# Kernel tuning notes

Measured on AMD Instinct MI355X. Metric: run time of the kernel, lower is better.

The kernel has to match this reference:

```python
import jax, jax.numpy as jnp
import numpy as np

M, U, H, C, EMB, HID = 4096, 8, 8, 64, 64, 128
N = M * U            # 32768 nodes
E = 131072           # edges
D = H * C            # 512 = heads * hidden_channels
NUM_LAYERS = 4
IN0 = 6              # 2 coords + mask + speed + cost + arrival
SCALE = np.float32(1.0 / np.sqrt(C))

def _lin(x, W, b):
    return x @ W + b

def _transformer_conv(x, src, dst, Wq, bq, Wk, bk, Wv, bv, Ws, bs):
    # PyG TransformerConv: x_j = x[src], x_i = x[dst]; softmax over edges per dst
    n = x.shape[0]
    q = _lin(x, Wq, bq).reshape(n, H, C)
    k = _lin(x, Wk, bk).reshape(n, H, C)
    v = _lin(x, Wv, bv).reshape(n, H, C)
    alpha = jnp.einsum('ehc,ehc->eh', q[dst], k[src]) * SCALE   # [E,H]
    amax = jax.ops.segment_max(alpha, dst, num_segments=n)       # [N,H]
    ex = jnp.exp(alpha - amax[dst])
    denom = jax.ops.segment_sum(ex, dst, num_segments=n)         # [N,H]
    agg = jax.ops.segment_sum(ex[:, :, None] * v[src], dst, num_segments=n)  # [N,H,C]
    out = agg / (denom[:, :, None] + 1e-16)
    return out.reshape(n, D) + _lin(x, Ws, bs)                   # concat heads + root skip

def _forward(mission_coords, uavs_info, speeds, cost_matrix, arrival_times,
             Wq0, bq0, Wk0, bk0, Wv0, bv0, Ws0, bs0,
             Wq, bq, Wk, bk, Wv, bv, Ws, bs,
             fc_W, fc_b, aW1, ab1, aW2, ab2, cW1, cb1, cW2, cb2,
             edge_index, batch, action_mask):
    mc = jnp.broadcast_to(mission_coords[:, None, :], (M, U, 2))
    mk = jnp.broadcast_to(action_mask[:, None, None].astype(jnp.float32), (M, U, 1))
    sp = jnp.broadcast_to(speeds[None, :, None], (M, U, 1))
    cm = cost_matrix.T[:, :, None]
    at = arrival_times.T[:, :, None]
    x = jnp.concatenate([mc, mk, sp, cm, at], axis=-1).reshape(N, IN0)
    src, dst = edge_index[0], edge_index[1]
    x = jax.nn.relu(_transformer_conv(x, src, dst, Wq0, bq0, Wk0, bk0, Wv0, bv0, Ws0, bs0))
    for l in range(NUM_LAYERS - 1):
        x = jax.nn.relu(_transformer_conv(x, src, dst, Wq[l], bq[l], Wk[l], bk[l], Wv[l], bv[l], Ws[l], bs[l]))
    new_batch = jnp.repeat(batch, U)                             # [N]
    sums = jax.ops.segment_sum(x, new_batch, num_segments=1)
    cnts = jax.ops.segment_sum(jnp.ones((N,), x.dtype), new_batch, num_segments=1)
    pooled = sums / cnts[:, None]                                # [1, D]
    emb = _lin(pooled, fc_W, fc_b)                               # [1, EMB]
    emb_exp = jnp.tile(emb, (U, 1))                              # [U, EMB]
    combined = jnp.concatenate([uavs_info, emb_exp, speeds[:, None]], axis=-1)  # [U, EMB+3]
    action_probs = jax.nn.softmax(_lin(jax.nn.relu(_lin(combined, aW1, ab1)), aW2, ab2), axis=-1)
    state_values = _lin(jax.nn.relu(_lin(combined, cW1, cb1)), cW2, cb2)
    return action_probs, state_values

def setup_inputs() -> dict:
    key = jax.random.key(0)
    ks = jax.random.split(key, 40)
    def nrm(i, shape, s=0.05):
        return jax.random.normal(ks[i], shape, jnp.float32) * s
    z = lambda *s: jnp.zeros(s, jnp.float32)
    L = NUM_LAYERS - 1
    inp = dict(
        mission_coords=jax.random.uniform(ks[0], (M, 2), jnp.float32),
        uavs_info=nrm(1, (U, 2), 1.0),
        speeds=jax.random.uniform(ks[2], (U,), jnp.float32) + 0.5,
        cost_matrix=jax.random.uniform(ks[3], (U, M), jnp.float32),
        arrival_times=jax.random.uniform(ks[4], (U, M), jnp.float32),
        edge_index=jax.random.randint(ks[5], (2, E), 0, N),
        batch=jnp.zeros((M,), jnp.int32),
        action_mask=jax.random.randint(ks[6], (M,), 0, 2),
        Wq0=nrm(7, (IN0, D)), bq0=z(D), Wk0=nrm(8, (IN0, D)), bk0=z(D),
        Wv0=nrm(9, (IN0, D)), bv0=z(D), Ws0=nrm(10, (IN0, D)), bs0=z(D),
        Wq=nrm(11, (L, D, D)), bq=z(L, D), Wk=nrm(12, (L, D, D)), bk=z(L, D),
        Wv=nrm(13, (L, D, D)), bv=z(L, D), Ws=nrm(14, (L, D, D)), bs=z(L, D),
        fc_W=nrm(15, (D, EMB)), fc_b=z(EMB),
        aW1=nrm(16, (EMB + 3, HID)), ab1=z(HID), aW2=nrm(17, (HID, M)), ab2=z(M),
        cW1=nrm(18, (EMB + 3, HID)), cb1=z(HID), cW2=nrm(19, (HID, 1)), cb2=z(1),
    )
    return inp

def reference(mission_coords, edge_index, batch, uavs_info, action_mask, speeds,
              cost_matrix, arrival_times,
              Wq0, bq0, Wk0, bk0, Wv0, bv0, Ws0, bs0,
              Wq, bq, Wk, bk, Wv, bv, Ws, bs,
              fc_W, fc_b, aW1, ab1, aW2, ab2, cW1, cb1, cW2, cb2):
    return _forward(mission_coords, uavs_info, speeds, cost_matrix, arrival_times,
                    Wq0, bq0, Wk0, bk0, Wv0, bv0, Ws0, bs0,
                    Wq, bq, Wk, bk, Wv, bv, Ws, bs,
                    fc_W, fc_b, aW1, ab1, aW2, ab2, cW1, cb1, cW2, cb2,
                    edge_index, batch, action_mask)
```

## Files before the change

### kernel.cpp

```cpp
#include <hip/hip_runtime.h>
#include <stdint.h>

typedef unsigned char u8;
typedef unsigned short u16;
typedef unsigned long long u64;
typedef __attribute__((ext_vector_type(8))) unsigned short u16x8;
typedef __attribute__((ext_vector_type(8))) __bf16 bf16x8;
typedef __attribute__((ext_vector_type(4))) float f32x4;
typedef __attribute__((ext_vector_type(2))) float f32x2;

#define NNODES 32768
#define NEDGES 131072
#define DDIM 512
#define QK4 2048
#define MM 4096
#define UU 8


__device__ __forceinline__ u16 f2bf(float f) {
    unsigned u = __builtin_bit_cast(unsigned, f);
    u += 0x7FFFu + ((u >> 16) & 1u);
    return (u16)(u >> 16);
}
__device__ __forceinline__ float bf2f(u16 h) {
    return __builtin_bit_cast(float, (unsigned)h << 16);
}
__device__ __forceinline__ void enc8(const float* f, int* lo, int* hi) {
    int a = __builtin_amdgcn_cvt_pk_fp8_f32(f[0], f[1], 0, false);
    a = __builtin_amdgcn_cvt_pk_fp8_f32(f[2], f[3], a, true);
    int b = __builtin_amdgcn_cvt_pk_fp8_f32(f[4], f[5], 0, false);
    b = __builtin_amdgcn_cvt_pk_fp8_f32(f[6], f[7], b, true);
    *lo = a;
    *hi = b;
}
__device__ __forceinline__ void dec8(int lo, int hi, float* f) {
    f32x2 a = __builtin_amdgcn_cvt_pk_f32_fp8(lo, false);
    f32x2 b = __builtin_amdgcn_cvt_pk_f32_fp8(lo, true);
    f32x2 c = __builtin_amdgcn_cvt_pk_f32_fp8(hi, false);
    f32x2 d = __builtin_amdgcn_cvt_pk_f32_fp8(hi, true);
    f[0] = a[0]; f[1] = a[1]; f[2] = b[0]; f[3] = b[1];
    f[4] = c[0]; f[5] = c[1]; f[6] = d[0]; f[7] = d[1];
}

__device__ __forceinline__ void load_lds16(const void* g, void* l) {
    __builtin_amdgcn_global_load_lds((__attribute__((address_space(1))) unsigned int*)(void*)g,
                                     (__attribute__((address_space(3))) unsigned int*)l, 16, 0, 0);
}

__global__ void k_prep(const float* __restrict__ mc, const int* __restrict__ mask,
                       const float* __restrict__ sp, const float* __restrict__ cm,
                       const float* __restrict__ at, float* __restrict__ x0,
                       const float* __restrict__ bq, const float* __restrict__ bk,
                       const float* __restrict__ bv, const float* __restrict__ bs,
                       float* __restrict__ bcat,
                       int* __restrict__ deg, float* __restrict__ pooled) {
    int b = blockIdx.x;
    int t = threadIdx.x;
    if (b < 128) {
        int node = b * 256 + t;
        deg[node] = 0;
        int m = node >> 3, u = node & 7;
        float* o = x0 + (size_t)node * 6;
        o[0] = mc[m * 2];
        o[1] = mc[m * 2 + 1];
        o[2] = (float)mask[m];
        o[3] = sp[u];
        o[4] = cm[u * MM + m];
        o[5] = at[u * MM + m];
    } else if (b < 152) {
        int i = (b - 128) * 256 + t;
        int n = i & (QK4 - 1);
        int l = i >> 11;
        const float* p;
        int col;
        if (n < 512) { p = bq; col = n; }
        else if (n < 1536) {
            int g = n - 512, c = g >> 4, r = g & 15;
            if (r < 8) { p = bk; col = c * 8 + r; }
            else { p = bv; col = c * 8 + r - 8; }
        } else { p = bs; col = n - 1536; }
        bcat[(size_t)l * QK4 + n] = p[l * DDIM + col];
    } else {
        pooled[(b - 152) * 256 + t] = 0.f;
    }
}

__global__ void k_c0(const float* __restrict__ Wq0, const float* __restrict__ bq0,
                     const float* __restrict__ Wk0, const float* __restrict__ bk0,
                     float* __restrict__ C0) {
    int i = threadIdx.x;
    if (i >= 392) return;
    int h = i / 49, r = i % 49;
    int d0 = h * 64;
    float s = 0.f;
    if (r < 36) {
        int a = r / 6, b = r % 6;
        for (int d = 0; d < 64; d++) s += Wq0[a * DDIM + d0 + d] * Wk0[b * DDIM + d0 + d];
    } else if (r < 42) {
        int a = r - 36;
        for (int d = 0; d < 64; d++) s += Wq0[a * DDIM + d0 + d] * bk0[d0 + d];
    } else if (r < 48) {
        int b = r - 42;
        for (int d = 0; d < 64; d++) s += Wk0[b * DDIM + d0 + d] * bq0[d0 + d];
    } else {
        for (int d = 0; d < 64; d++) s += bq0[d0 + d] * bk0[d0 + d];
    }
    C0[i] = s;
}

__global__ void k_wt(const float* __restrict__ Wq, const float* __restrict__ Wk,
                     const float* __restrict__ Wv, const float* __restrict__ Ws,
                     u16* __restrict__ Wt) {
    __shared__ float tile[32][33];
    int q = blockIdx.z;
    int l = q >> 2, t = q & 3;
    const float* src = ((t == 0) ? Wq : (t == 1) ? Wk : (t == 2) ? Wv : Ws) + (size_t)l * DDIM * DDIM;
    int k0 = blockIdx.x * 32, n0 = blockIdx.y * 32;
    int tx = threadIdx.x, ty = threadIdx.y;
#pragma unroll
    for (int r = 0; r < 4; r++) tile[ty + 8 * r][tx] = src[(size_t)(k0 + ty + 8 * r) * DDIM + n0 + tx];
    __syncthreads();
    u16* dst = Wt + (size_t)l * QK4 * DDIM;
#pragma unroll
    for (int r = 0; r < 4; r++) {
        int nn = n0 + ty + 8 * r;
        int n;
        if (t == 0) n = nn;
        else if (t == 1) n = 512 + ((nn >> 3) << 4) + (nn & 7);
        else if (t == 2) n = 512 + ((nn >> 3) << 4) + 8 + (nn & 7);
        else n = 1536 + nn;
        dst[(size_t)n * DDIM + k0 + tx] = f2bf(tile[tx][ty + 8 * r]);
    }
}

__global__ void k_count(const int* __restrict__ dst, int* __restrict__ deg) {
    int e = blockIdx.x * 256 + threadIdx.x;
    if (e < NEDGES) atomicAdd(&deg[dst[e]], 1);
}

__global__ __launch_bounds__(1024) void k_scan(const int* __restrict__ deg, int* __restrict__ offs,
                                               int* __restrict__ cursor) {
    __shared__ int sums[1024];
    int t = threadIdx.x;
    int base = t * 32;
    int local[32];
    int s = 0;
#pragma unroll
    for (int i = 0; i < 32; i++) { local[i] = s; s += deg[base + i]; }
    sums[t] = s;
    __syncthreads();
    for (int d = 1; d < 1024; d <<= 1) {
        int v = (t >= d) ? sums[t - d] : 0;
        __syncthreads();
        sums[t] += v;
        __syncthreads();
    }
    int excl = (t == 0) ? 0 : sums[t - 1];
#pragma unroll
    for (int i = 0; i < 32; i++) {
        int o = excl + local[i];
        offs[base + i] = o;
        cursor[base + i] = o;
    }
    if (t == 1023) offs[NNODES] = sums[1023];
}

__global__ void k_scatter(const int* __restrict__ src, const int* __restrict__ dst,
                          int* __restrict__ cursor, int* __restrict__ ssrc) {
    int e = blockIdx.x * 256 + threadIdx.x;
    if (e < NEDGES) {
        int pos = atomicAdd(&cursor[dst[e]], 1);
        ssrc[pos] = src[e];
    }
}

__global__ __launch_bounds__(256) void k_attn0(const float* __restrict__ x0, const float* __restrict__ C0,
                                               const float* __restrict__ Wv0, const float* __restrict__ bv0,
                                               const float* __restrict__ Ws0, const float* __restrict__ bs0,
                                               const int* __restrict__ offs, const int* __restrict__ ssrc,
                                               u16* __restrict__ Xout) {
    const int lane = threadIdx.x & 63;
    const int wv = threadIdx.x >> 6;
    const int g = lane >> 3;
    const int h = lane & 7;
    float wV[8][6], wS[8][6], bV[8], bS[8];
#pragma unroll
    for (int j = 0; j < 8; ++j) {
        int c = lane + 64 * j;
        bV[j] = bv0[c];
        bS[j] = bs0[c];
#pragma unroll
        for (int a = 0; a < 6; ++a) {
            wV[j][a] = Wv0[a * DDIM + c];
            wS[j][a] = Ws0[a * DDIM + c];
        }
    }
    float Ah[36], uh[6], wh[6], ch;
#pragma unroll
    for (int r = 0; r < 36; ++r) Ah[r] = C0[h * 49 + r];
#pragma unroll
    for (int a = 0; a < 6; ++a) uh[a] = C0[h * 49 + 36 + a];
#pragma unroll
    for (int a = 0; a < 6; ++a) wh[a] = C0[h * 49 + 42 + a];
    ch = C0[h * 49 + 48];

    const int node0 = (blockIdx.x * 4 + wv) * 8;
    const int node = node0 + g;
    float xi[6];
#pragma unroll
    for (int a = 0; a < 6; ++a) xi[a] = x0[(size_t)node * 6 + a];
    const int e0 = offs[node];
    const int deg = offs[node + 1] - e0;
    int dmax = deg;
    dmax = max(dmax, __shfl_xor(dmax, 8, 64));
    dmax = max(dmax, __shfl_xor(dmax, 16, 64));
    dmax = max(dmax, __shfl_xor(dmax, 32, 64));

    float m = -1e30f, l = 0.f;
    float xh[6];
#pragma unroll
    for (int a = 0; a < 6; ++a) xh[a] = 0.f;
    float xj[6];
    {
        int s = (deg > 0) ? ssrc[e0] : 0;
#pragma unroll
        for (int a = 0; a < 6; ++a) xj[a] = x0[(size_t)s * 6 + a];
    }
    for (int e = 0; e < dmax; ++e) {
        float xc[6];
#pragma unroll
        for (int a = 0; a < 6; ++a) xc[a] = xj[a];
        const bool act = (e < deg);
        int sn = (e + 1 < deg) ? ssrc[e0 + e + 1] : 0;
#pragma unroll
        for (int a = 0; a < 6; ++a) xj[a] = x0[(size_t)sn * 6 + a];
        float alpha = ch;
#pragma unroll
        for (int a = 0; a < 6; ++a) {
            float t = uh[a];
#pragma unroll
            for (int b = 0; b < 6; ++b) t += Ah[a * 6 + b] * xc[b];
            alpha += xi[a] * t;
        }
#pragma unroll
        for (int b = 0; b < 6; ++b) alpha += wh[b] * xc[b];
        alpha *= 0.125f;
        float nm = act ? fmaxf(m, alpha) : m;
        float corr = __expf(m - nm);
        float p = act ? __expf(alpha - nm) : 0.f;
        l = l * corr + p;
#pragma unroll
        for (int a = 0; a < 6; ++a) xh[a] = xh[a] * corr + p * xc[a];
        m = nm;
    }
#pragma unroll
    for (int nn = 0; nn < 8; ++nn) {
        int dnode = node0 + nn;
        float xin[6];
#pragma unroll
        for (int a = 0; a < 6; ++a) xin[a] = __shfl(xi[a], nn * 8, 64);
#pragma unroll
        for (int j = 0; j < 8; ++j) {
            int srcl = nn * 8 + j;
            float lb = __shfl(l, srcl, 64);
            float num = lb * bV[j];
#pragma unroll
            for (int a = 0; a < 6; ++a) num += __shfl(xh[a], srcl, 64) * wV[j][a];
            float skip = bS[j];
#pragma unroll
            for (int a = 0; a < 6; ++a) skip += xin[a] * wS[j][a];
            float r = num / (lb + 1e-16f) + skip;
            Xout[(size_t)dnode * DDIM + lane + 64 * j] = f2bf(fmaxf(r, 0.f));
        }
    }
}

__global__ __launch_bounds__(256, 4) void k_gemm(const u16* __restrict__ X, const u16* __restrict__ Wt,
                                                 const float* __restrict__ bcat, u8* __restrict__ Q8,
                                                 u8* __restrict__ KV8, u16* __restrict__ S16) {
    __shared__ __align__(16) u16 smem[2 * 128 * 64];
    u16* As = smem;
    u16* Bs = smem + 128 * 64;
    const int tid = threadIdx.x;
    const int lane = tid & 63;
    const int w = tid >> 6;
    const int wm = w & 1, wn = w >> 1;
    const int bid = blockIdx.x;
    const int xcd = bid & 7;
    const int s = bid >> 3;
    const size_t arow0 = (size_t)(xcd * 32 + (s >> 4)) * 128;
    const size_t brow0 = (size_t)(s & 15) * 128;
    const int bt = (int)(brow0 >> 7);

    f32x4 acc[4][4];
#pragma unroll
    for (int i = 0; i < 4; i++)
#pragma unroll
        for (int j = 0; j < 4; j++) acc[i][j] = (f32x4){0.f, 0.f, 0.f, 0.f};

    const int la = lane & 7;
    const int quad = lane >> 4;
    const int lm = lane & 15;

    for (int kt = 0; kt < 8; ++kt) {
        const int k0 = kt * 64;
#pragma unroll
        for (int t = 0; t < 4; ++t) {
            int idx = (w * 4 + t) * 64 + lane;
            int m = idx >> 3;
            int c = la ^ (m & 7);
            const u16* ga = X + (arow0 + m) * DDIM + (k0 + c * 8);
            const u16* gb = Wt + (brow0 + m) * DDIM + (k0 + c * 8);
            load_lds16(ga, &As[(size_t)((w * 4 + t) * 64) * 8]);
            load_lds16(gb, &Bs[(size_t)((w * 4 + t) * 64) * 8]);
        }
        __syncthreads();
#pragma unroll
        for (int kk = 0; kk < 2; ++kk) {
            bf16x8 af[4], bfg[4];
            int c = kk * 4 + quad;
#pragma unroll
            for (int i = 0; i < 4; ++i) {
                int m = wm * 64 + i * 16 + lm;
                int slot = m * 8 + (c ^ (m & 7));
                af[i] = *(const bf16x8*)&As[(size_t)slot * 8];
            }
#pragma unroll
            for (int j = 0; j < 4; ++j) {
                int n = wn * 64 + j * 16 + lm;
                int slot = n * 8 + (c ^ (n & 7));
                bfg[j] = *(const bf16x8*)&Bs[(size_t)slot * 8];
            }
#pragma unroll
            for (int i = 0; i < 4; ++i)
#pragma unroll
                for (int j = 0; j < 4; ++j)
                    acc[i][j] = __builtin_amdgcn_mfma_f32_16x16x32_bf16(af[i], bfg[j], acc[i][j], 0, 0, 0);
        }
        __syncthreads();
    }

    float biasv[4];
#pragma unroll
    for (int j = 0; j < 4; ++j) biasv[j] = bcat[brow0 + wn * 64 + j * 16 + lm];

    u16* stg = smem;
    const int chunk = lane & 7;
    const int rrow = lane >> 3;
    const int colbase = (int)brow0 + wn * 64 + chunk * 8;
#pragma unroll
    for (int p = 0; p < 2; ++p) {
        __syncthreads();
#pragma unroll
        for (int ii = 0; ii < 2; ++ii) {
            int i = p * 2 + ii;
#pragma unroll
            for (int j = 0; j < 4; ++j) {
#pragma unroll
                for (int r = 0; r < 4; ++r) {
                    int lr = ii * 16 + quad * 4 + r;
                    int lc = j * 16 + lm;
                    stg[(size_t)(w * 32 + lr) * 72 + lc] = f2bf(acc[i][j][r] + biasv[j]);
                }
            }
        }
        __syncthreads();
#pragma unroll
        for (int it = 0; it < 4; ++it) {
            int row = it * 8 + rrow;
            u16x8 v = *(const u16x8*)&stg[(size_t)(w * 32 + row) * 72 + chunk * 8];
            size_t grow = arow0 + wm * 64 + p * 32 + row;
            if (bt < 4) {
                float f[8];
#pragma unroll
                for (int j = 0; j < 8; j++) f[j] = bf2f(v[j]);
                int lo, hi;
                enc8(f, &lo, &hi);
                *(int2*)(Q8 + grow * 512 + colbase) = make_int2(lo, hi);
            } else if (bt < 12) {
                float f[8];
#pragma unroll
                for (int j = 0; j < 8; j++) f[j] = bf2f(v[j]);
                int lo, hi;
                enc8(f, &lo, &hi);
                *(int2*)(KV8 + grow * 1024 + (colbase - 512)) = make_int2(lo, hi);
            } else {
                *(u16x8*)(S16 + grow * 512 + (colbase - 1536)) = v;
            }
        }
    }
}

__global__ __launch_bounds__(256) void k_attn(const u8* __restrict__ Q8, const u8* __restrict__ KV8,
                                              const u16* __restrict__ S16, const int* __restrict__ offs,
                                              const int* __restrict__ ssrc, u16* __restrict__ Xout) {
    const int lane = threadIdx.x & 63;
    const int node = blockIdx.x * 4 + (threadIdx.x >> 6);
    const u64 q8 = *(const u64*)(Q8 + (size_t)node * 512 + (size_t)lane * 8);
    const u16x8 sv = *(const u16x8*)(S16 + (size_t)node * 512 + (size_t)lane * 8);
    float qf[8];
    dec8((int)(q8 & 0xFFFFFFFFull), (int)(q8 >> 32), qf);
    float m = -INFINITY, l = 0.f;
    float acc[8];
#pragma unroll
    for (int j = 0; j < 8; j++) acc[j] = 0.f;
    const int e0 = offs[node], e1 = offs[node + 1];
    int e = e0;
    while (e < e1) {
        int nb = e1 - e;
        if (nb > 4) nb = 4;
        int4 kvb[4];
#pragma unroll
        for (int i = 0; i < 4; ++i) {
            if (i < nb) {
                int s = ssrc[e + i];
                kvb[i] = *(const int4*)(KV8 + (size_t)s * 1024 + (size_t)lane * 16);
            }
        }
#pragma unroll
        for (int i = 0; i < 4; ++i) {
            if (i >= nb) break;
            int4 kv = kvb[i];
            f32x2 k01 = __builtin_amdgcn_cvt_pk_f32_fp8(kv.x, false);
            f32x2 k23 = __builtin_amdgcn_cvt_pk_f32_fp8(kv.x, true);
            f32x2 k45 = __builtin_amdgcn_cvt_pk_f32_fp8(kv.y, false);
            f32x2 k67 = __builtin_amdgcn_cvt_pk_f32_fp8(kv.y, true);
            float d = qf[0] * k01[0] + qf[1] * k01[1] + qf[2] * k23[0] + qf[3] * k23[1] +
                      qf[4] * k45[0] + qf[5] * k45[1] + qf[6] * k67[0] + qf[7] * k67[1];
            d += __shfl_xor(d, 1, 64);
            d += __shfl_xor(d, 2, 64);
            d += __shfl_xor(d, 4, 64);
            float a = d * 0.125f;
            float nm = fmaxf(m, a);
            float corr = __expf(m - nm);
            float p = __expf(a - nm);
            l = l * corr + p;
            f32x2 v01 = __builtin_amdgcn_cvt_pk_f32_fp8(kv.z, false);
            f32x2 v23 = __builtin_amdgcn_cvt_pk_f32_fp8(kv.z, true);
            f32x2 v45 = __builtin_amdgcn_cvt_pk_f32_fp8(kv.w, false);
            f32x2 v67 = __builtin_amdgcn_cvt_pk_f32_fp8(kv.w, true);
            acc[0] = acc[0] * corr + p * v01[0];
            acc[1] = acc[1] * corr + p * v01[1];
            acc[2] = acc[2] * corr + p * v23[0];
            acc[3] = acc[3] * corr + p * v23[1];
            acc[4] = acc[4] * corr + p * v45[0];
            acc[5] = acc[5] * corr + p * v45[1];
            acc[6] = acc[6] * corr + p * v67[0];
            acc[7] = acc[7] * corr + p * v67[1];
            m = nm;
        }
        e += nb;
    }
    float inv = 1.0f / (l + 1e-16f);
    u16x8 o;
#pragma unroll
    for (int j = 0; j < 8; j++) {
        float r = acc[j] * inv + bf2f(sv[j]);
        o[j] = f2bf(fmaxf(r, 0.f));
    }
    *(u16x8*)(Xout + (size_t)node * DDIM + (size_t)lane * 8) = o;
}

__global__ __launch_bounds__(256) void k_pool(const u16* __restrict__ X, float* __restrict__ pooled) {
    __shared__ float red[4][64][8];
    int t = threadIdx.x;
    int chunk = t & 63;
    int rofs = t >> 6;
    float s[8];
#pragma unroll
    for (int j = 0; j < 8; j++) s[j] = 0.f;
    int nd0 = blockIdx.x * 256;
    for (int nd = nd0 + rofs; nd < nd0 + 256; nd += 4) {
        u16x8 v = *(const u16x8*)&X[(size_t)nd * DDIM + chunk * 8];
#pragma unroll
        for (int j = 0; j < 8; j++) s[j] += bf2f(v[j]);
    }
#pragma unroll
    for (int j = 0; j < 8; j++) red[rofs][chunk][j] = s[j];
    __syncthreads();
    if (t < 64) {
#pragma unroll
        for (int j = 0; j < 8; j++) {
            float o = red[0][t][j] + red[1][t][j] + red[2][t][j] + red[3][t][j];
            atomicAdd(&pooled[t * 8 + j], o);
        }
    }
}

__global__ __launch_bounds__(1024) void k_heads(const float* __restrict__ pooled, const float* __restrict__ fcW,
                                                const float* __restrict__ fcb, const float* __restrict__ ui,
                                                const float* __restrict__ sp, const float* __restrict__ aW1,
                                                const float* __restrict__ ab1, const float* __restrict__ cW1,
                                                const float* __restrict__ cb1, const float* __restrict__ cW2,
                                                const float* __restrict__ cb2, float* __restrict__ hidden_a,
                                                float* __restrict__ out) {
    __shared__ float spool[512];
    __shared__ float semb[64];
    __shared__ float shc[8][128];
    int t = threadIdx.x;
    if (t < 512) spool[t] = pooled[t] * (1.0f / 32768.0f);
    __syncthreads();
    if (t < 64) {
        float s = fcb[t];
        for (int k = 0; k < 512; k++) s += spool[k] * fcW[k * 64 + t];
        semb[t] = s;
    }
    __syncthreads();
    int u = t >> 7, j = t & 127;
    float u0 = ui[u * 2], u1 = ui[u * 2 + 1], uspd = sp[u];
    float ha = ab1[j] + u0 * aW1[j] + u1 * aW1[128 + j] + uspd * aW1[66 * 128 + j];
    float hc = cb1[j] + u0 * cW1[j] + u1 * cW1[128 + j] + uspd * cW1[66 * 128 + j];
    for (int k = 0; k < 64; k++) {
        float e = semb[k];
        ha += e * aW1[(2 + k) * 128 + j];
        hc += e * cW1[(2 + k) * 128 + j];
    }
    ha = fmaxf(ha, 0.f);
    hc = fmaxf(hc, 0.f);
    hidden_a[u * 128 + j] = ha;
    shc[u][j] = hc;
    __syncthreads();
    if (t < 8) {
        float s = cb2[0];
        for (int k = 0; k < 128; k++) s += shc[t][k] * cW2[k];
        out[NNODES + t] = s;
    }
}

__global__ __launch_bounds__(1024) void k_actor(const float* __restrict__ hidden_a, const float* __restrict__ aW2,
                                                const float* __restrict__ ab2, float* __restrict__ out) {
    __shared__ float h[128];
    __shared__ float red[1024];
    int u = blockIdx.x, t = threadIdx.x;
    if (t < 128) h[t] = hidden_a[u * 128 + t];
    __syncthreads();
    float lg[4];
#pragma unroll
    for (int p = 0; p < 4; p++) {
        int mcol = t + p * 1024;
        float s = ab2[mcol];
        for (int k = 0; k < 128; k++) s += h[k] * aW2[(size_t)k * MM + mcol];
        lg[p] = s;
    }
    float mx = fmaxf(fmaxf(lg[0], lg[1]), fmaxf(lg[2], lg[3]));
    red[t] = mx;
    __syncthreads();
    for (int s2 = 512; s2 > 0; s2 >>= 1) {
        if (t < s2) red[t] = fmaxf(red[t], red[t + s2]);
        __syncthreads();
    }
    mx = red[0];
    __syncthreads();
    float e[4], sum = 0.f;
#pragma unroll
    for (int p = 0; p < 4; p++) {
        e[p] = __expf(lg[p] - mx);
        sum += e[p];
    }
    red[t] = sum;
    __syncthreads();
    for (int s2 = 512; s2 > 0; s2 >>= 1) {
        if (t < s2) red[t] += red[t + s2];
        __syncthreads();
    }
    float inv = 1.0f / red[0];
#pragma unroll
    for (int p = 0; p < 4; p++) out[(size_t)u * MM + t + p * 1024] = e[p] * inv;
}

extern "C" void kernel_launch(void* const* d_in, const int* in_sizes, int n_in,
                              void* d_out, int out_size, void* d_ws, size_t ws_size,
                              hipStream_t stream) {
    const float* mc   = (const float*)d_in[0];
    const float* ui   = (const float*)d_in[1];
    const float* sp   = (const float*)d_in[2];
    const float* cm   = (const float*)d_in[3];
    const float* at   = (const float*)d_in[4];
    const int*   eidx = (const int*)d_in[5];
    const int*   mask = (const int*)d_in[7];
    const float* Wq0 = (const float*)d_in[8];
    const float* bq0 = (const float*)d_in[9];
    const float* Wk0 = (const float*)d_in[10];
    const float* bk0 = (const float*)d_in[11];
    const float* Wv0 = (const float*)d_in[12];
    const float* bv0 = (const float*)d_in[13];
    const float* Ws0 = (const float*)d_in[14];
    const float* bs0 = (const float*)d_in[15];
    const float* Wq = (const float*)d_in[16];
    const float* bq = (const float*)d_in[17];
    const float* Wk = (const float*)d_in[18];
    const float* bk = (const float*)d_in[19];
    const float* Wv = (const float*)d_in[20];
    const float* bv = (const float*)d_in[21];
    const float* Ws = (const float*)d_in[22];
    const float* bs = (const float*)d_in[23];
    const float* fcW = (const float*)d_in[24];
    const float* fcb = (const float*)d_in[25];
    const float* aW1 = (const float*)d_in[26];
    const float* ab1 = (const float*)d_in[27];
    const float* aW2 = (const float*)d_in[28];
    const float* ab2 = (const float*)d_in[29];
    const float* cW1 = (const float*)d_in[30];
    const float* cb1 = (const float*)d_in[31];
    const float* cW2 = (const float*)d_in[32];
    const float* cb2 = (const float*)d_in[33];
    float* out = (float*)d_out;

    const int* esrc = eidx;
    const int* edst = eidx + NEDGES;

    char* ws = (char*)d_ws;
    size_t off = 0;
    auto alloc = [&](size_t bytes) -> void* {
        void* p = ws + off;
        off += (bytes + 255) & ~(size_t)255;
        return p;
    };
    u8*    Q8    = (u8*)alloc((size_t)NNODES * 512);
    u8*    KV8   = (u8*)alloc((size_t)NNODES * 1024);
    u16*   S16   = (u16*)alloc((size_t)NNODES * 512 * 2);
    u16*   X     = (u16*)alloc((size_t)NNODES * DDIM * 2);
    u16*   Wt    = (u16*)alloc((size_t)3 * QK4 * DDIM * 2);
    float* bcat  = (float*)alloc((size_t)3 * QK4 * 4);
    float* C0    = (float*)alloc((size_t)392 * 4);
    float* x0    = (float*)alloc((size_t)NNODES * 6 * 4);
    int*   deg   = (int*)alloc((size_t)NNODES * 4);
    int*   offs  = (int*)alloc((size_t)(NNODES + 1) * 4);
    int*   cursor= (int*)alloc((size_t)NNODES * 4);
    int*   ssrc  = (int*)alloc((size_t)NEDGES * 4);
    float* pooled= (float*)alloc((size_t)512 * 4);
    float* hidden_a = (float*)alloc((size_t)UU * 128 * 4);
    (void)ws_size; (void)in_sizes; (void)n_in; (void)out_size;

    k_prep<<<154, 256, 0, stream>>>(mc, mask, sp, cm, at, x0, bq, bk, bv, bs, bcat, deg, pooled);
    k_c0<<<1, 512, 0, stream>>>(Wq0, bq0, Wk0, bk0, C0);
    {
        dim3 g(16, 16, 12), b(32, 8);
        k_wt<<<g, b, 0, stream>>>(Wq, Wk, Wv, Ws, Wt);
    }
    k_count<<<NEDGES / 256, 256, 0, stream>>>(edst, deg);
    k_scan<<<1, 1024, 0, stream>>>(deg, offs, cursor);
    k_scatter<<<NEDGES / 256, 256, 0, stream>>>(esrc, edst, cursor, ssrc);

    k_attn0<<<1024, 256, 0, stream>>>(x0, C0, Wv0, bv0, Ws0, bs0, offs, ssrc, X);

    for (int l = 0; l < 3; ++l) {
        k_gemm<<<4096, 256, 0, stream>>>(X, Wt + (size_t)l * QK4 * DDIM, bcat + (size_t)l * QK4, Q8, KV8, S16);
        k_attn<<<NNODES / 4, 256, 0, stream>>>(Q8, KV8, S16, offs, ssrc, X);
    }

    k_pool<<<128, 256, 0, stream>>>(X, pooled);
    k_heads<<<1, 1024, 0, stream>>>(pooled, fcW, fcb, ui, sp, aW1, ab1, cW1, cb1, cW2, cb2, hidden_a, out);
    k_actor<<<UU, 1024, 0, stream>>>(hidden_a, aW2, ab2, out);
}
```

Measured before the change: 594.0 us.

## Merge setup kernels into k_prep and batch edge-index loads in attention

Folds the C0 precompute and the weight transpose/bf16 conversion kernels into the single k_prep launch, so two kernel launches go away. In k_attn, each wavefront now loads up to 64 neighbour indices with one coalesced load and broadcasts them with shuffles, and it issues 8 KV gathers in flight per batch instead of 4. This targets launch overhead and the latency of dependent index-then-gather loads, at the cost of more registers for the wider KV buffer.

```diff
diff --git a/kernel.cpp b/kernel.cpp
--- a/kernel.cpp
+++ b/kernel.cpp
@@ -53,7 +53,14 @@
                        const float* __restrict__ bq, const float* __restrict__ bk,
                        const float* __restrict__ bv, const float* __restrict__ bs,
                        float* __restrict__ bcat,
-                       int* __restrict__ deg, float* __restrict__ pooled) {
+                       int* __restrict__ deg, float* __restrict__ pooled,
+                       const float* __restrict__ Wq0, const float* __restrict__ bq0,
+                       const float* __restrict__ Wk0, const float* __restrict__ bk0,
+                       float* __restrict__ C0,
+                       const float* __restrict__ Wq, const float* __restrict__ Wk,
+                       const float* __restrict__ Wv, const float* __restrict__ Ws,
+                       u16* __restrict__ Wt) {
+    __shared__ float tile[32][33];
     int b = blockIdx.x;
     int t = threadIdx.x;
     if (b < 128) {
@@ -80,56 +87,50 @@
             else { p = bv; col = c * 8 + r - 8; }
         } else { p = bs; col = n - 1536; }
         bcat[(size_t)l * QK4 + n] = p[l * DDIM + col];
+    } else if (b < 154) {
+        pooled[(b - 152) * 256 + t] = 0.f;
+    } else if (b < 156) {
+        int i = (b - 154) * 256 + t;
+        if (i < 392) {
+            int h = i / 49, r = i % 49;
+            int d0 = h * 64;
+            float s = 0.f;
+            if (r < 36) {
+                int a = r / 6, bb = r % 6;
+                for (int d = 0; d < 64; d++) s += Wq0[a * DDIM + d0 + d] * Wk0[bb * DDIM + d0 + d];
+            } else if (r < 42) {
+                int a = r - 36;
+                for (int d = 0; d < 64; d++) s += Wq0[a * DDIM + d0 + d] * bk0[d0 + d];
+            } else if (r < 48) {
+                int bb = r - 42;
+                for (int d = 0; d < 64; d++) s += Wk0[bb * DDIM + d0 + d] * bq0[d0 + d];
+            } else {
+                for (int d = 0; d < 64; d++) s += bq0[d0 + d] * bk0[d0 + d];
+            }
+            C0[i] = s;
+        }
     } else {
-        pooled[(b - 152) * 256 + t] = 0.f;
-    }
-}
-
-__global__ void k_c0(const float* __restrict__ Wq0, const float* __restrict__ bq0,
-                     const float* __restrict__ Wk0, const float* __restrict__ bk0,
-                     float* __restrict__ C0) {
-    int i = threadIdx.x;
-    if (i >= 392) return;
-    int h = i / 49, r = i % 49;
-    int d0 = h * 64;
-    float s = 0.f;
-    if (r < 36) {
-        int a = r / 6, b = r % 6;
-        for (int d = 0; d < 64; d++) s += Wq0[a * DDIM + d0 + d] * Wk0[b * DDIM + d0 + d];
-    } else if (r < 42) {
-        int a = r - 36;
-        for (int d = 0; d < 64; d++) s += Wq0[a * DDIM + d0 + d] * bk0[d0 + d];
-    } else if (r < 48) {
-        int b = r - 42;
-        for (int d = 0; d < 64; d++) s += Wk0[b * DDIM + d0 + d] * bq0[d0 + d];
-    } else {
-        for (int d = 0; d < 64; d++) s += bq0[d0 + d] * bk0[d0 + d];
-    }
-    C0[i] = s;
-}
-
-__global__ void k_wt(const float* __restrict__ Wq, const float* __restrict__ Wk,
-                     const float* __restrict__ Wv, const float* __restrict__ Ws,
-                     u16* __restrict__ Wt) {
-    __shared__ float tile[32][33];
-    int q = blockIdx.z;
-    int l = q >> 2, t = q & 3;
-    const float* src = ((t == 0) ? Wq : (t == 1) ? Wk : (t == 2) ? Wv : Ws) + (size_t)l * DDIM * DDIM;
-    int k0 = blockIdx.x * 32, n0 = blockIdx.y * 32;
-    int tx = threadIdx.x, ty = threadIdx.y;
-#pragma unroll
-    for (int r = 0; r < 4; r++) tile[ty + 8 * r][tx] = src[(size_t)(k0 + ty + 8 * r) * DDIM + n0 + tx];
-    __syncthreads();
-    u16* dst = Wt + (size_t)l * QK4 * DDIM;
-#pragma unroll
-    for (int r = 0; r < 4; r++) {
-        int nn = n0 + ty + 8 * r;
-        int n;
-        if (t == 0) n = nn;
-        else if (t == 1) n = 512 + ((nn >> 3) << 4) + (nn & 7);
-        else if (t == 2) n = 512 + ((nn >> 3) << 4) + 8 + (nn & 7);
-        else n = 1536 + nn;
-        dst[(size_t)n * DDIM + k0 + tx] = f2bf(tile[tx][ty + 8 * r]);
+        int bb = b - 156;
+        int q = bb >> 8;
+        int rr = bb & 255;
+        int l = q >> 2, ty4 = q & 3;
+        const float* src = ((ty4 == 0) ? Wq : (ty4 == 1) ? Wk : (ty4 == 2) ? Wv : Ws) + (size_t)l * DDIM * DDIM;
+        int k0 = (rr >> 4) * 32, n0 = (rr & 15) * 32;
+        int tx = t & 31, ty = t >> 5;
+#pragma unroll
+        for (int r = 0; r < 4; r++) tile[ty + 8 * r][tx] = src[(size_t)(k0 + ty + 8 * r) * DDIM + n0 + tx];
+        __syncthreads();
+        u16* dst = Wt + (size_t)l * QK4 * DDIM;
+#pragma unroll
+        for (int r = 0; r < 4; r++) {
+            int nn = n0 + ty + 8 * r;
+            int n;
+            if (ty4 == 0) n = nn;
+            else if (ty4 == 1) n = 512 + ((nn >> 3) << 4) + (nn & 7);
+            else if (ty4 == 2) n = 512 + ((nn >> 3) << 4) + 8 + (nn & 7);
+            else n = 1536 + nn;
+            dst[(size_t)n * DDIM + k0 + tx] = f2bf(tile[tx][ty + 8 * r]);
+        }
     }
 }
 
@@ -405,51 +406,55 @@
 #pragma unroll
     for (int j = 0; j < 8; j++) acc[j] = 0.f;
     const int e0 = offs[node], e1 = offs[node + 1];
-    int e = e0;
-    while (e < e1) {
-        int nb = e1 - e;
-        if (nb > 4) nb = 4;
-        int4 kvb[4];
-#pragma unroll
-        for (int i = 0; i < 4; ++i) {
-            if (i < nb) {
-                int s = ssrc[e + i];
-                kvb[i] = *(const int4*)(KV8 + (size_t)s * 1024 + (size_t)lane * 16);
+    const int deg = e1 - e0;
+    for (int base = 0; base < deg; base += 64) {
+        int cnt = deg - base;
+        if (cnt > 64) cnt = 64;
+        int idx = (lane < cnt) ? ssrc[e0 + base + lane] : 0;
+        for (int b = 0; b < cnt; b += 8) {
+            int nb = cnt - b;
+            if (nb > 8) nb = 8;
+            int4 kvb[8];
+#pragma unroll
+            for (int i = 0; i < 8; ++i) {
+                if (i < nb) {
+                    int s = __shfl(idx, b + i, 64);
+                    kvb[i] = *(const int4*)(KV8 + (size_t)s * 1024 + (size_t)lane * 16);
+                }
             }
-        }
-#pragma unroll
-        for (int i = 0; i < 4; ++i) {
-            if (i >= nb) break;
-            int4 kv = kvb[i];
-            f32x2 k01 = __builtin_amdgcn_cvt_pk_f32_fp8(kv.x, false);
-            f32x2 k23 = __builtin_amdgcn_cvt_pk_f32_fp8(kv.x, true);
-            f32x2 k45 = __builtin_amdgcn_cvt_pk_f32_fp8(kv.y, false);
-            f32x2 k67 = __builtin_amdgcn_cvt_pk_f32_fp8(kv.y, true);
-            float d = qf[0] * k01[0] + qf[1] * k01[1] + qf[2] * k23[0] + qf[3] * k23[1] +
-                      qf[4] * k45[0] + qf[5] * k45[1] + qf[6] * k67[0] + qf[7] * k67[1];
-            d += __shfl_xor(d, 1, 64);
-            d += __shfl_xor(d, 2, 64);
-            d += __shfl_xor(d, 4, 64);
-            float a = d * 0.125f;
-            float nm = fmaxf(m, a);
-            float corr = __expf(m - nm);
-            float p = __expf(a - nm);
-            l = l * corr + p;
-            f32x2 v01 = __builtin_amdgcn_cvt_pk_f32_fp8(kv.z, false);
-            f32x2 v23 = __builtin_amdgcn_cvt_pk_f32_fp8(kv.z, true);
-            f32x2 v45 = __builtin_amdgcn_cvt_pk_f32_fp8(kv.w, false);
-            f32x2 v67 = __builtin_amdgcn_cvt_pk_f32_fp8(kv.w, true);
-            acc[0] = acc[0] * corr + p * v01[0];
-            acc[1] = acc[1] * corr + p * v01[1];
-            acc[2] = acc[2] * corr + p * v23[0];
-            acc[3] = acc[3] * corr + p * v23[1];
-            acc[4] = acc[4] * corr + p * v45[0];
-            acc[5] = acc[5] * corr + p * v45[1];
-            acc[6] = acc[6] * corr + p * v67[0];
-            acc[7] = acc[7] * corr + p * v67[1];
-            m = nm;
-        }
-        e += nb;
+#pragma unroll
+            for (int i = 0; i < 8; ++i) {
+                if (i >= nb) break;
+                int4 kv = kvb[i];
+                f32x2 k01 = __builtin_amdgcn_cvt_pk_f32_fp8(kv.x, false);
+                f32x2 k23 = __builtin_amdgcn_cvt_pk_f32_fp8(kv.x, true);
+                f32x2 k45 = __builtin_amdgcn_cvt_pk_f32_fp8(kv.y, false);
+                f32x2 k67 = __builtin_amdgcn_cvt_pk_f32_fp8(kv.y, true);
+                float d = qf[0] * k01[0] + qf[1] * k01[1] + qf[2] * k23[0] + qf[3] * k23[1] +
+                          qf[4] * k45[0] + qf[5] * k45[1] + qf[6] * k67[0] + qf[7] * k67[1];
+                d += __shfl_xor(d, 1, 64);
+                d += __shfl_xor(d, 2, 64);
+                d += __shfl_xor(d, 4, 64);
+                float a = d * 0.125f;
+                float nm = fmaxf(m, a);
+                float corr = __expf(m - nm);
+                float p = __expf(a - nm);
+                l = l * corr + p;
+                f32x2 v01 = __builtin_amdgcn_cvt_pk_f32_fp8(kv.z, false);
+                f32x2 v23 = __builtin_amdgcn_cvt_pk_f32_fp8(kv.z, true);
+                f32x2 v45 = __builtin_amdgcn_cvt_pk_f32_fp8(kv.w, false);
+                f32x2 v67 = __builtin_amdgcn_cvt_pk_f32_fp8(kv.w, true);
+                acc[0] = acc[0] * corr + p * v01[0];
+                acc[1] = acc[1] * corr + p * v01[1];
+                acc[2] = acc[2] * corr + p * v23[0];
+                acc[3] = acc[3] * corr + p * v23[1];
+                acc[4] = acc[4] * corr + p * v45[0];
+                acc[5] = acc[5] * corr + p * v45[1];
+                acc[6] = acc[6] * corr + p * v67[0];
+                acc[7] = acc[7] * corr + p * v67[1];
+                m = nm;
+            }
+        }
     }
     float inv = 1.0f / (l + 1e-16f);
     u16x8 o;
@@ -632,12 +637,8 @@
     float* hidden_a = (float*)alloc((size_t)UU * 128 * 4);
     (void)ws_size; (void)in_sizes; (void)n_in; (void)out_size;
 
-    k_prep<<<154, 256, 0, stream>>>(mc, mask, sp, cm, at, x0, bq, bk, bv, bs, bcat, deg, pooled);
-    k_c0<<<1, 512, 0, stream>>>(Wq0, bq0, Wk0, bk0, C0);
-    {
-        dim3 g(16, 16, 12), b(32, 8);
-        k_wt<<<g, b, 0, stream>>>(Wq, Wk, Wv, Ws, Wt);
-    }
+    k_prep<<<3228, 256, 0, stream>>>(mc, mask, sp, cm, at, x0, bq, bk, bv, bs, bcat, deg, pooled,
+                                     Wq0, bq0, Wk0, bk0, C0, Wq, Wk, Wv, Ws, Wt);
     k_count<<<NEDGES / 256, 256, 0, stream>>>(edst, deg);
     k_scan<<<1, 1024, 0, stream>>>(deg, offs, cursor);
     k_scatter<<<NEDGES / 256, 256, 0, stream>>>(esrc, edst, cursor, ssrc);
```

Result: slower. 631.3 us (+6.3%).
